# Kernel optimization log

Hardware: AMD Instinct MI355X
Metric: run time of the kernel (lower is better)

## Reference

```python
import jax, jax.numpy as jnp
import numpy as np

B, LQ, LK = 2, 2048, 77
DIM, XDIM = 320, 768
H, HD = 8, 40  # heads, head_dim; DIM == H*HD
FF = 4 * DIM  # GEGLU inner dim


def _ln(x, g, b, eps=1e-5):
    m = x.mean(-1, keepdims=True)
    v = ((x - m) ** 2).mean(-1, keepdims=True)
    return (x - m) * jax.lax.rsqrt(v + eps) * g + b


def _split_heads(x):  # [B,L,DIM] -> [B,H,L,HD]
    return x.reshape(x.shape[0], x.shape[1], H, HD).transpose(0, 2, 1, 3)


def _merge_heads(x):  # [B,H,L,HD] -> [B,L,DIM]
    return x.transpose(0, 2, 1, 3).reshape(x.shape[0], x.shape[2], H * HD)


def setup_inputs() -> dict:
    key = jax.random.key(0)
    ks = jax.random.split(key, 24)
    s = 0.02
    r = lambda i, shp: s * jax.random.normal(ks[i], shp, jnp.float32)
    return {
        "hidden_states": jax.random.normal(ks[0], (B, LQ, DIM), jnp.float32),
        "encoder_hidden_states": jax.random.normal(ks[1], (B, LK, XDIM), jnp.float32),
        # norm1 + self-attn (attn1)
        "ln1_g": jnp.ones((DIM,), jnp.float32), "ln1_b": jnp.zeros((DIM,), jnp.float32),
        "wq1": r(2, (DIM, DIM)), "wk1": r(3, (DIM, DIM)), "wv1": r(4, (DIM, DIM)),
        "wo1": r(5, (DIM, DIM)), "bo1": jnp.zeros((DIM,), jnp.float32),
        # norm2 + Hadamard cross-attn (attn2)
        "ln2_g": jnp.ones((DIM,), jnp.float32), "ln2_b": jnp.zeros((DIM,), jnp.float32),
        "wq2": r(6, (DIM, DIM)), "wk2": r(7, (XDIM, DIM)), "wvh": r(8, (DIM, DIM)),
        "wo2": r(9, (DIM, DIM)), "bo2": jnp.zeros((DIM,), jnp.float32),
        # norm3 + GEGLU feed-forward
        "ln3_g": jnp.ones((DIM,), jnp.float32), "ln3_b": jnp.zeros((DIM,), jnp.float32),
        "wff1": r(10, (DIM, 2 * FF)), "bff1": jnp.zeros((2 * FF,), jnp.float32),
        "wff2": r(11, (FF, DIM)), "bff2": jnp.zeros((DIM,), jnp.float32),
    }


def reference(hidden_states, encoder_hidden_states, ln1_g, ln1_b, wq1, wk1, wv1,
              wo1, bo1, ln2_g, ln2_b, wq2, wk2, wvh, wo2, bo2, ln3_g, ln3_b,
              wff1, bff1, wff2, bff2):
    scale = 1.0 / jnp.sqrt(jnp.asarray(HD, hidden_states.dtype))

    # ---- self-attention (SDPA semantics) ----
    h = _ln(hidden_states, ln1_g, ln1_b)
    q = _split_heads(h @ wq1)
    k = _split_heads(h @ wk1)
    v = _split_heads(h @ wv1)
    scores = jnp.einsum('bhqd,bhkd->bhqk', q, k) * scale
    w = jax.nn.softmax(scores, axis=-1)
    attn = jnp.einsum('bhqk,bhkd->bhqd', w, v)
    attn = _merge_heads(attn) @ wo1 + bo1
    hidden_states = hidden_states + attn

    # ---- Hadamard cross-attention: value comes from hidden_states (len Lq) ----
    h = _ln(hidden_states, ln2_g, ln2_b)
    q = _split_heads(h @ wq2)                     # [B,H,Lq,HD]
    k = _split_heads(encoder_hidden_states @ wk2) # [B,H,Lk,HD]
    vH = _split_heads(h @ wvh)                    # [B,H,Lq,HD]
    scores = jnp.einsum('bhqd,bhkd->bhqk', q, k) * scale
    w = jax.nn.softmax(scores, axis=-1)           # [B,H,Lq,Lk]
    # (w[...,None] * vH[...,None,:]).sum(-2) == vH * w.sum(-1, keepdims) (v indep of k)
    cross = vH * jnp.sum(w, axis=-1, keepdims=True)
    cross = _merge_heads(cross) @ wo2 + bo2
    hidden_states = hidden_states + cross

    # ---- GEGLU feed-forward ----
    h = _ln(hidden_states, ln3_g, ln3_b)
    proj = h @ wff1 + bff1
    x, gate = jnp.split(proj, 2, axis=-1)
    ff = (x * jax.nn.gelu(gate, approximate=False)) @ wff2 + bff2
    return hidden_states + ff
```

## Files before the change

### kernel.cpp

```cpp
#include <hip/hip_runtime.h>
#include <math.h>

#define DIM   320
#define HD    40
#define NH    8
#define LQ    2048
#define BATCH 2
#define MROWS 4096
#define FFD   1280
#define FF2   2560

#define KSPLIT 8
#define KCHUNK (LQ/KSPLIT)
#define KT     32
#define NT     (KCHUNK/KT)
#define NQROWS (BATCH*NH*LQ)

#define LSCALE (0.15811388300841897f * 1.4426950408889634f)

typedef unsigned short ushort_t;
typedef unsigned int u32;
using bf16x8 = __attribute__((ext_vector_type(8))) short;
using f32x4  = __attribute__((ext_vector_type(4))) float;

static __device__ inline ushort_t f2bf(float f) {
  union { float f; unsigned u; } x{f};
  unsigned r = x.u + 0x7FFFu + ((x.u >> 16) & 1u);
  return (ushort_t)(r >> 16);
}
static __device__ inline float bf2f(ushort_t h) {
  union { unsigned u; float f; } x; x.u = ((unsigned)h) << 16; return x.f;
}

__global__ __launch_bounds__(256) void ln_kernel(
    const float* __restrict__ X, const float* __restrict__ g,
    const float* __restrict__ bta, ushort_t* __restrict__ Y)
{
  int row  = blockIdx.x * 4 + (threadIdx.x >> 6);
  int lane = threadIdx.x & 63;
  const float* x = X + (size_t)row * DIM;
  float v[5];
  float s = 0.f;
#pragma unroll
  for (int i = 0; i < 5; ++i) { v[i] = x[lane + 64*i]; s += v[i]; }
#pragma unroll
  for (int off = 32; off >= 1; off >>= 1) s += __shfl_xor(s, off, 64);
  float mean = s * (1.0f/DIM);
  float sq = 0.f;
#pragma unroll
  for (int i = 0; i < 5; ++i) { float d = v[i] - mean; sq += d*d; }
#pragma unroll
  for (int off = 32; off >= 1; off >>= 1) sq += __shfl_xor(sq, off, 64);
  float rstd = rsqrtf(sq*(1.0f/DIM) + 1e-5f);
  ushort_t* y = Y + (size_t)row * DIM;
#pragma unroll
  for (int i = 0; i < 5; ++i) {
    int c = lane + 64*i;
    y[c] = f2bf((v[i]-mean)*rstd*g[c] + bta[c]);
  }
}

#define OFF_WQKVT 0
#define OFF_WO1T  (960*320)
#define OFF_WO2T  (OFF_WO1T + 320*320)
#define OFF_WFF1T (OFF_WO2T + 320*320)
#define OFF_WFF2T (OFF_WFF1T + 320*2560)
#define OFF_WVHB  (OFF_WFF2T + 1280*320)
#define WBF_TOTAL (OFF_WVHB + 320*320)

__global__ __launch_bounds__(256) void convw_kernel(
    const float* __restrict__ wq1, const float* __restrict__ wk1,
    const float* __restrict__ wv1, const float* __restrict__ wo1,
    const float* __restrict__ wo2, const float* __restrict__ wff1,
    const float* __restrict__ wff2, const float* __restrict__ wvh,
    ushort_t* __restrict__ dst)
{
  int e = blockIdx.y;
  const float* src; int K, N; size_t doff; int tr = 1; float scale = 1.f;
  switch (e) {
    case 0: src=wq1;  K=320;  N=320;  doff=OFF_WQKVT; scale=LSCALE; break;
    case 1: src=wk1;  K=320;  N=320;  doff=OFF_WQKVT + 320*320;  break;
    case 2: src=wv1;  K=320;  N=320;  doff=OFF_WQKVT + 2*320*320;break;
    case 3: src=wo1;  K=320;  N=320;  doff=OFF_WO1T;             break;
    case 4: src=wo2;  K=320;  N=320;  doff=OFF_WO2T;             break;
    case 5: src=wff1; K=320;  N=2560; doff=OFF_WFF1T;            break;
    case 6: src=wff2; K=1280; N=320;  doff=OFF_WFF2T;            break;
    default: src=wvh; K=320;  N=320;  doff=OFF_WVHB; tr=0;       break;
  }
  int ntN = N/32;
  int nt_total = (K/32)*ntN;
  int t = blockIdx.x;
  if (t >= nt_total) return;
  int kt = t / ntN, nt = t - kt*ntN;
  __shared__ float tile[32][33];
  int tx = threadIdx.x & 31, ty = threadIdx.x >> 5;
  ushort_t* d = dst + doff;
#pragma unroll
  for (int i = 0; i < 4; ++i) {
    int r = ty + 8*i;
    tile[r][tx] = src[(size_t)(kt*32+r)*N + nt*32+tx] * scale;
  }
  __syncthreads();
  if (tr) {
#pragma unroll
    for (int i = 0; i < 4; ++i) {
      int r = ty + 8*i;
      d[(size_t)(nt*32+r)*K + kt*32+tx] = f2bf(tile[tx][r]);
    }
  } else {
#pragma unroll
    for (int i = 0; i < 4; ++i) {
      int r = ty + 8*i;
      d[(size_t)(kt*32+r)*N + nt*32+tx] = f2bf(tile[r][tx]);
    }
  }
}

__global__ __launch_bounds__(256) void vt_kernel(
    const ushort_t* __restrict__ qkv, ushort_t* __restrict__ Vimg,
    ushort_t* __restrict__ Kimg)
{
  int bh = blockIdx.y;
  int kt = blockIdx.x;
  int b = bh >> 3, h = bh & 7;
  int tid = threadIdx.x;
  __shared__ ushort_t tile[64*42];

  const ushort_t* ksrc = qkv + (size_t)(b*LQ + kt*64)*960 + DIM + h*HD;
  ushort_t* kdst = Kimg + ((size_t)bh*64 + kt*2)*2048;
#pragma unroll
  for (int i = 0; i < 2; ++i) {
    int f = i*256 + tid;
    if (f < 320) {
      int r = f/5, s = f - 5*r;
      int t_ = r >> 5, rr = r & 31;
      int c = s ^ (rr & 7);
      *(uint4*)(kdst + (size_t)t_*2048 + rr*64 + c*8) =
          *(const uint4*)(ksrc + (size_t)r*960 + s*8);
    }
  }
  if (tid < 192) {
    int r = tid/3, s = tid - 3*r;
    int t_ = r >> 5, rr = r & 31;
    int c = (5+s) ^ (rr & 7);
    uint4 z = {0,0,0,0};
    *(uint4*)(kdst + (size_t)t_*2048 + rr*64 + c*8) = z;
  }

  const ushort_t* vsrc = qkv + (size_t)(b*LQ + kt*64)*960 + 2*DIM + h*HD;
#pragma unroll
  for (int i = 0; i < 5; ++i) {
    int f = i*256 + tid;
    int r = f/20, c2 = f - r*20;
    *(unsigned*)(tile + r*42 + c2*2) = *(const unsigned*)(vsrc + (size_t)r*960 + c2*2);
  }
  __syncthreads();
  ushort_t* vdst = Vimg + ((size_t)bh*64 + kt*2)*1536;
#pragma unroll
  for (int i = 0; i < 6; ++i) {
    int f = i*256 + tid;
    int dd = f >> 5, kk = f & 31;
    unsigned val = 0;
    if (dd < 40) {
      unsigned lo = tile[(kk*2)*42 + dd];
      unsigned hi = tile[(kk*2+1)*42 + dd];
      val = lo | (hi << 16);
    }
    int t_ = kk >> 4, p = kk & 15;
    int c = (p >> 2) ^ (dd & 3);
    *(unsigned*)(vdst + (size_t)t_*1536 + dd*32 + c*8 + (p&3)*2) = val;
  }
}

#define AST 72
__global__ __launch_bounds__(256) void mgemm(
    const ushort_t* __restrict__ A, int lda,
    const ushort_t* __restrict__ Bt, int ldb,
    const float* __restrict__ bias,
    const float* __restrict__ R,
    float* __restrict__ Cf, ushort_t* __restrict__ Cb, int ldc,
    int K)
{
  __shared__ ushort_t As[64*AST];
  __shared__ ushort_t Bs[64*AST];
  int tid = threadIdx.x;
  int w = tid >> 6, lane = tid & 63, quad = lane >> 4, n16 = lane & 15;
  int wm = w >> 1, wn = w & 1;
  int bm = blockIdx.y * 64, bn = blockIdx.x * 64;
  int sr = tid >> 2, sc = (tid & 3) << 4;
  const ushort_t* Ag = A  + (size_t)(bm + sr)*lda + sc;
  const ushort_t* Bg = Bt + (size_t)(bn + sr)*ldb + sc;

  f32x4 acc00 = {0.f,0.f,0.f,0.f}, acc01 = acc00, acc10 = acc00, acc11 = acc00;

  float4 av0 = *(const float4*)(Ag);
  float4 av1 = *(const float4*)(Ag + 8);
  float4 bv0 = *(const float4*)(Bg);
  float4 bv1 = *(const float4*)(Bg + 8);
  for (int k0 = 0; k0 < K; k0 += 64) {
    __syncthreads();
    *(float4*)(As + sr*AST + sc)     = av0;
    *(float4*)(As + sr*AST + sc + 8) = av1;
    *(float4*)(Bs + sr*AST + sc)     = bv0;
    *(float4*)(Bs + sr*AST + sc + 8) = bv1;
    __syncthreads();
    if (k0 + 64 < K) {
      av0 = *(const float4*)(Ag + k0 + 64);
      av1 = *(const float4*)(Ag + k0 + 72);
      bv0 = *(const float4*)(Bg + k0 + 64);
      bv1 = *(const float4*)(Bg + k0 + 72);
    }
#pragma unroll
    for (int kk = 0; kk < 64; kk += 32) {
      bf16x8 fa0 = *(const bf16x8*)(As + (wm*32 +      n16)*AST + kk + quad*8);
      bf16x8 fa1 = *(const bf16x8*)(As + (wm*32 + 16 + n16)*AST + kk + quad*8);
      bf16x8 fb0 = *(const bf16x8*)(Bs + (wn*32 +      n16)*AST + kk + quad*8);
      bf16x8 fb1 = *(const bf16x8*)(Bs + (wn*32 + 16 + n16)*AST + kk + quad*8);
      acc00 = __builtin_amdgcn_mfma_f32_16x16x32_bf16(fa0, fb0, acc00, 0,0,0);
      acc01 = __builtin_amdgcn_mfma_f32_16x16x32_bf16(fa0, fb1, acc01, 0,0,0);
      acc10 = __builtin_amdgcn_mfma_f32_16x16x32_bf16(fa1, fb0, acc10, 0,0,0);
      acc11 = __builtin_amdgcn_mfma_f32_16x16x32_bf16(fa1, fb1, acc11, 0,0,0);
    }
  }

  f32x4 accs[2][2] = {{acc00, acc01},{acc10, acc11}};
#pragma unroll
  for (int s = 0; s < 2; ++s)
#pragma unroll
    for (int t = 0; t < 2; ++t) {
      int c = bn + wn*32 + t*16 + n16;
      float bb = bias ? bias[c] : 0.f;
#pragma unroll
      for (int i = 0; i < 4; ++i) {
        int r = bm + wm*32 + s*16 + quad*4 + i;
        float v = accs[s][t][i] + bb;
        if (R)  v += R[(size_t)r*ldc + c];
        if (Cf) Cf[(size_t)r*ldc + c] = v;
        if (Cb) Cb[(size_t)r*ldc + c] = f2bf(v);
      }
    }
}

#define AS_STRIDE 40
__global__ __launch_bounds__(256) void mgemm128(
    const ushort_t* __restrict__ A, int lda,
    const ushort_t* __restrict__ Bt, int ldb,
    ushort_t* __restrict__ Cb, int ldc, int K)
{
  __shared__ ushort_t As[128*AS_STRIDE];
  __shared__ ushort_t Bs[64*AS_STRIDE];
  int tid = threadIdx.x;
  int w = tid >> 6, lane = tid & 63, quad = lane >> 4, n16 = lane & 15;
  int wm = w >> 1, wn = w & 1;
  int bm = blockIdx.y * 128, bn = blockIdx.x * 64;
  int ar = tid >> 1, ac = (tid & 1) << 4;
  int br = tid >> 2, bc = (tid & 3) << 3;
  const ushort_t* Ag = A  + (size_t)(bm + ar)*lda + ac;
  const ushort_t* Bg = Bt + (size_t)(bn + br)*ldb + bc;

  f32x4 acc[4][2];
#pragma unroll
  for (int s = 0; s < 4; ++s)
#pragma unroll
    for (int t = 0; t < 2; ++t) acc[s][t] = f32x4{0.f,0.f,0.f,0.f};

  float4 av0 = *(const float4*)(Ag);
  float4 av1 = *(const float4*)(Ag + 8);
  float4 bv  = *(const float4*)(Bg);
  for (int k0 = 0; k0 < K; k0 += 32) {
    __syncthreads();
    *(float4*)(As + ar*AS_STRIDE + ac)     = av0;
    *(float4*)(As + ar*AS_STRIDE + ac + 8) = av1;
    *(float4*)(Bs + br*AS_STRIDE + bc)     = bv;
    __syncthreads();
    if (k0 + 32 < K) {
      av0 = *(const float4*)(Ag + k0 + 32);
      av1 = *(const float4*)(Ag + k0 + 40);
      bv  = *(const float4*)(Bg + k0 + 32);
    }
    bf16x8 fa[4], fb[2];
#pragma unroll
    for (int s = 0; s < 4; ++s)
      fa[s] = *(const bf16x8*)(As + (wm*64 + s*16 + n16)*AS_STRIDE + quad*8);
#pragma unroll
    for (int t = 0; t < 2; ++t)
      fb[t] = *(const bf16x8*)(Bs + (wn*32 + t*16 + n16)*AS_STRIDE + quad*8);
#pragma unroll
    for (int s = 0; s < 4; ++s)
#pragma unroll
      for (int t = 0; t < 2; ++t)
        acc[s][t] = __builtin_amdgcn_mfma_f32_16x16x32_bf16(fa[s], fb[t], acc[s][t], 0,0,0);
  }

#pragma unroll
  for (int s = 0; s < 4; ++s)
#pragma unroll
    for (int t = 0; t < 2; ++t) {
      int c = bn + wn*32 + t*16 + n16;
#pragma unroll
      for (int i = 0; i < 4; ++i) {
        int r = bm + wm*64 + s*16 + quad*4 + i;
        Cb[(size_t)r*ldc + c] = f2bf(acc[s][t][i]);
      }
    }
}

__global__ __launch_bounds__(256) void ff1_geglu(
    const ushort_t* __restrict__ A, const ushort_t* __restrict__ Bt,
    const float* __restrict__ bias, ushort_t* __restrict__ Og)
{
  __shared__ ushort_t As[128*AS_STRIDE];
  __shared__ ushort_t Bxs[64*AS_STRIDE];
  __shared__ ushort_t Bgs[64*AS_STRIDE];
  int tid = threadIdx.x;
  int w = tid >> 6, lane = tid & 63, quad = lane >> 4, n16 = lane & 15;
  int wm = w >> 1, wn = w & 1;
  int bm = blockIdx.y * 128, bn = blockIdx.x * 64;
  int ar = tid >> 1, ac = (tid & 1) << 4;
  int br = tid >> 2, bc = (tid & 3) << 3;
  const ushort_t* Ag  = A  + (size_t)(bm + ar)*DIM + ac;
  const ushort_t* Bxg = Bt + (size_t)(bn + br)*DIM + bc;
  const ushort_t* Bgg = Bt + (size_t)(bn + FFD + br)*DIM + bc;

  f32x4 ax[4][2], ag[4][2];
#pragma unroll
  for (int s = 0; s < 4; ++s)
#pragma unroll
    for (int t = 0; t < 2; ++t) { ax[s][t] = f32x4{0.f,0.f,0.f,0.f}; ag[s][t] = ax[s][t]; }

  float4 av0 = *(const float4*)(Ag);
  float4 av1 = *(const float4*)(Ag + 8);
  float4 bxv = *(const float4*)(Bxg);
  float4 bgv = *(const float4*)(Bgg);
  for (int k0 = 0; k0 < DIM; k0 += 32) {
    __syncthreads();
    *(float4*)(As  + ar*AS_STRIDE + ac)     = av0;
    *(float4*)(As  + ar*AS_STRIDE + ac + 8) = av1;
    *(float4*)(Bxs + br*AS_STRIDE + bc)     = bxv;
    *(float4*)(Bgs + br*AS_STRIDE + bc)     = bgv;
    __syncthreads();
    if (k0 + 32 < DIM) {
      av0 = *(const float4*)(Ag  + k0 + 32);
      av1 = *(const float4*)(Ag  + k0 + 40);
      bxv = *(const float4*)(Bxg + k0 + 32);
      bgv = *(const float4*)(Bgg + k0 + 32);
    }
    bf16x8 fa[4], fx[2], fg[2];
#pragma unroll
    for (int s = 0; s < 4; ++s)
      fa[s] = *(const bf16x8*)(As + (wm*64 + s*16 + n16)*AS_STRIDE + quad*8);
#pragma unroll
    for (int t = 0; t < 2; ++t) {
      fx[t] = *(const bf16x8*)(Bxs + (wn*32 + t*16 + n16)*AS_STRIDE + quad*8);
      fg[t] = *(const bf16x8*)(Bgs + (wn*32 + t*16 + n16)*AS_STRIDE + quad*8);
    }
#pragma unroll
    for (int s = 0; s < 4; ++s)
#pragma unroll
      for (int t = 0; t < 2; ++t) {
        ax[s][t] = __builtin_amdgcn_mfma_f32_16x16x32_bf16(fa[s], fx[t], ax[s][t], 0,0,0);
        ag[s][t] = __builtin_amdgcn_mfma_f32_16x16x32_bf16(fa[s], fg[t], ag[s][t], 0,0,0);
      }
  }

  const float kk = 0.7071067811865476f;
#pragma unroll
  for (int s = 0; s < 4; ++s)
#pragma unroll
    for (int t = 0; t < 2; ++t) {
      int c = bn + wn*32 + t*16 + n16;
      float bx = bias[c], bg = bias[c + FFD];
#pragma unroll
      for (int i = 0; i < 4; ++i) {
        int r = bm + wm*64 + s*16 + quad*4 + i;
        float xx = ax[s][t][i] + bx;
        float gg = ag[s][t][i] + bg;
        Og[(size_t)r*FFD + c] = f2bf(xx * 0.5f * gg * (1.f + erff(gg * kk)));
      }
    }
}

#define TILE_K_SH 2048
#define TILE_V_SH 1536
#define TILE_SH   (TILE_K_SH + TILE_V_SH)

__global__ __launch_bounds__(256, 2) void attn_mfma(
    const ushort_t* __restrict__ qkv, const ushort_t* __restrict__ Kimg,
    const ushort_t* __restrict__ Vimg,
    float* __restrict__ Pl, ushort_t* __restrict__ Pacc)
{
  __shared__ ushort_t lds[2*TILE_SH];
  int tid  = threadIdx.x;
  int w    = tid >> 6;
  int lane = tid & 63;
  int quad = lane >> 4;
  int n16  = lane & 15;

  int blk  = blockIdx.x;
  int bh   = (blk & 7) | (((blk >> 3) & 1) << 3);
  int rest = blk >> 4;
  int qt   = rest & 15;
  int ks   = rest >> 4;
  int b = bh >> 3, h = bh & 7;

  const ushort_t* qrowa = qkv + (size_t)(b*LQ + qt*128 + w*32 + n16)*960 + h*HD;
  const ushort_t* qrowb = qrowa + 16*960;
  bf16x8 qf0a = *(const bf16x8*)(qrowa + quad*8);
  bf16x8 qf1a = *(const bf16x8*)(qrowa + 32);
  bf16x8 qf0b = *(const bf16x8*)(qrowb + quad*8);
  bf16x8 qf1b = *(const bf16x8*)(qrowb + 32);

  const ushort_t* Ktb = Kimg + ((size_t)bh*64 + ks*NT)*TILE_K_SH;
  const ushort_t* Vtb = Vimg + ((size_t)bh*64 + ks*NT)*TILE_V_SH;

  int swk0 = (quad ^ (n16 & 7)) << 3;
  int swk1 = ((quad + 4) ^ (n16 & 7)) << 3;
  int kof0 = n16*64 + swk0;
  int kof1 = n16*64 + swk1;
  int kof2 = (16+n16)*64 + swk0;
  int kof3 = (16+n16)*64 + swk1;
  int swv  = (quad ^ (n16 & 3)) << 3;
  int vof0 = n16*32 + swv;
  int vof1 = (16+n16)*32 + swv;
  int vof2 = (32+n16)*32 + swv;

  f32x4 o0a = {0.f,0.f,0.f,0.f}, o1a = o0a, o2a = o0a;
  f32x4 o0b = o0a, o1b = o0a, o2b = o0a;
  f32x4 la0a = o0a, la1a = o0a, la0b = o0a, la1b = o0a;

#define CVTPK(D, LO, HI) \
  asm("v_cvt_pk_bf16_f32 %0, %1, %2" : "=v"(D) : "v"(LO), "v"(HI))
#define PSWAP32(X, Y) \
  asm("v_permlane32_swap_b32 %0, %1" : "+v"(X), "+v"(Y))
#define PSWAP16(X, Y) \
  asm("v_permlane16_swap_b32 %0, %1" : "+v"(X), "+v"(Y))

#define STAGE(BUF, T) { \
  const ushort_t* ks_ = Ktb + (size_t)(T)*TILE_K_SH + w*512 + lane*8; \
  ushort_t* kd_ = lds + (BUF)*TILE_SH + w*512; \
  __builtin_amdgcn_global_load_lds( \
      (const __attribute__((address_space(1))) u32*)ks_, \
      (__attribute__((address_space(3))) u32*)kd_, 16, 0, 0); \
  if (w < 3) { \
    const ushort_t* vs_ = Vtb + (size_t)(T)*TILE_V_SH + w*512 + lane*8; \
    ushort_t* vd_ = lds + (BUF)*TILE_SH + TILE_K_SH + w*512; \
    __builtin_amdgcn_global_load_lds( \
        (const __attribute__((address_space(1))) u32*)vs_, \
        (__attribute__((address_space(3))) u32*)vd_, 16, 0, 0); \
  } }

#define HALF(Q0F, Q1F, LA0, LA1, FRAG) \
  bf16x8 FRAG; { \
  f32x4 st0 = {-8.f,-8.f,-8.f,-8.f}; f32x4 st1 = st0; \
  st0 = __builtin_amdgcn_mfma_f32_16x16x32_bf16(K00, Q0F, st0, 0,0,0); \
  st1 = __builtin_amdgcn_mfma_f32_16x16x32_bf16(K10, Q0F, st1, 0,0,0); \
  st0 = __builtin_amdgcn_mfma_f32_16x16x32_bf16(K01, Q1F, st0, 0,0,0); \
  st1 = __builtin_amdgcn_mfma_f32_16x16x32_bf16(K11, Q1F, st1, 0,0,0); \
  f32x4 p0, p1; \
  _Pragma("unroll") \
  for (int r = 0; r < 4; ++r) { p0[r] = exp2f(st0[r]); p1[r] = exp2f(st1[r]); } \
  LA0 += p0; LA1 += p1; \
  unsigned d0, d1, d2, d3; \
  CVTPK(d0, p0[0], p0[1]); CVTPK(d1, p0[2], p0[3]); \
  CVTPK(d2, p1[0], p1[1]); CVTPK(d3, p1[2], p1[3]); \
  PSWAP32(d0, d2); PSWAP16(d0, d2);   \
  PSWAP32(d1, d3); PSWAP16(d1, d3);   \
  union { unsigned u[4]; bf16x8 v; } fr_; \
  fr_.u[0] = d0; fr_.u[1] = d1; fr_.u[2] = d2; fr_.u[3] = d3; \
  FRAG = fr_.v; }

  STAGE(0, 0);
  __syncthreads();
  for (int t = 0; t < NT; ++t) {
    int buf = t & 1;
    if (t + 1 < NT) STAGE(buf^1, t+1);
    const ushort_t* Kb_ = lds + buf*TILE_SH;
    const ushort_t* Vb_ = Kb_ + TILE_K_SH;
    bf16x8 K00 = *(const bf16x8*)(Kb_ + kof0);
    bf16x8 K01 = *(const bf16x8*)(Kb_ + kof1);
    bf16x8 K10 = *(const bf16x8*)(Kb_ + kof2);
    bf16x8 K11 = *(const bf16x8*)(Kb_ + kof3);
    bf16x8 V0  = *(const bf16x8*)(Vb_ + vof0);
    bf16x8 V1  = *(const bf16x8*)(Vb_ + vof1);
    bf16x8 V2  = *(const bf16x8*)(Vb_ + vof2);
    HALF(qf0a, qf1a, la0a, la1a, fragA)
    HALF(qf0b, qf1b, la0b, la1b, fragB)
    o0a = __builtin_amdgcn_mfma_f32_16x16x32_bf16(fragA, V0, o0a, 0,0,0);
    o0b = __builtin_amdgcn_mfma_f32_16x16x32_bf16(fragB, V0, o0b, 0,0,0);
    o1a = __builtin_amdgcn_mfma_f32_16x16x32_bf16(fragA, V1, o1a, 0,0,0);
    o1b = __builtin_amdgcn_mfma_f32_16x16x32_bf16(fragB, V1, o1b, 0,0,0);
    o2a = __builtin_amdgcn_mfma_f32_16x16x32_bf16(fragA, V2, o2a, 0,0,0);
    o2b = __builtin_amdgcn_mfma_f32_16x16x32_bf16(fragB, V2, o2b, 0,0,0);
    __syncthreads();
  }
#undef STAGE
#undef HALF
#undef CVTPK
#undef PSWAP32
#undef PSWAP16
// ... 52 lines not shown
    ushort_t ob[8];
#pragma unroll
    for (int j = 0; j < 8; ++j) ob[j] = f2bf(acc[j]*inv);
    *(uint4*)(orow + u*8) = *(uint4*)ob;
  }
}

extern "C" void kernel_launch(void* const* d_in, const int* in_sizes, int n_in,
                              void* d_out, int out_size, void* d_ws, size_t ws_size,
                              hipStream_t stream) {
  const float* hidden = (const float*)d_in[0];
  const float* ln1_g = (const float*)d_in[2];
  const float* ln1_b = (const float*)d_in[3];
  const float* wq1   = (const float*)d_in[4];
  const float* wk1   = (const float*)d_in[5];
  const float* wv1   = (const float*)d_in[6];
  const float* wo1   = (const float*)d_in[7];
  const float* bo1   = (const float*)d_in[8];
  const float* ln2_g = (const float*)d_in[9];
  const float* ln2_b = (const float*)d_in[10];
  const float* wvh   = (const float*)d_in[13];
  const float* wo2   = (const float*)d_in[14];
  const float* bo2   = (const float*)d_in[15];
  const float* ln3_g = (const float*)d_in[16];
  const float* ln3_b = (const float*)d_in[17];
  const float* wff1  = (const float*)d_in[18];
  const float* bff1  = (const float*)d_in[19];
  const float* wff2  = (const float*)d_in[20];
  const float* bff2  = (const float*)d_in[21];
  float* out = (float*)d_out;

  ushort_t* wsu = (ushort_t*)d_ws;
  ushort_t* wbf   = wsu;
  ushort_t* lnb   = wbf + WBF_TOTAL;
  ushort_t* qkvb  = lnb + (size_t)MROWS*DIM;
  ushort_t* attnb = qkvb + (size_t)MROWS*3*DIM;
  ushort_t* gegb  = attnb + (size_t)MROWS*DIM;
  ushort_t* wct   = gegb + (size_t)MROWS*FFD;
  ushort_t* vtb   = wct + 320*320;
  ushort_t* kpb   = vtb + (size_t)16*64*1536;
  ushort_t* Pacc  = kpb + (size_t)16*64*2048;
  float* fws = (float*)(Pacc + (size_t)KSPLIT*NQROWS*40 + 64);
  float* h1   = fws;
  float* h2   = h1 + (size_t)MROWS*DIM;
  float* Pl   = h2 + (size_t)MROWS*DIM;

  dim3 t256(256);
  dim3 gconv(800, 8);
  dim3 gqkv(15, 32);
  dim3 g320(5, 64);
  dim3 gwc(5, 5);
  dim3 gffg(20, 32);
  dim3 gvt(32, 16);
  dim3 gattn(16*16*KSPLIT);

  convw_kernel<<<gconv, t256, 0, stream>>>(wq1, wk1, wv1, wo1, wo2, wff1, wff2, wvh, wbf);
  mgemm<<<gwc, t256, 0, stream>>>(wbf + OFF_WO2T, DIM, wbf + OFF_WVHB, DIM,
                                  nullptr, nullptr, nullptr, wct, DIM, DIM);

  ln_kernel<<<MROWS/4, t256, 0, stream>>>(hidden, ln1_g, ln1_b, lnb);
  mgemm128<<<gqkv, t256, 0, stream>>>(lnb, DIM, wbf + OFF_WQKVT, DIM,
                                      qkvb, 3*DIM, DIM);
  vt_kernel<<<gvt, t256, 0, stream>>>(qkvb, vtb, kpb);
  attn_mfma<<<gattn, t256, 0, stream>>>(qkvb, kpb, vtb, Pl, Pacc);
  attn_merge<<<NQROWS/256, t256, 0, stream>>>(Pl, Pacc, attnb);
  mgemm<<<g320, t256, 0, stream>>>(attnb, DIM, wbf + OFF_WO1T, DIM, bo1, hidden,
                                   h1, nullptr, DIM, DIM);

  ln_kernel<<<MROWS/4, t256, 0, stream>>>(h1, ln2_g, ln2_b, lnb);
  mgemm<<<g320, t256, 0, stream>>>(lnb, DIM, wct, DIM, bo2, h1,
                                   h2, nullptr, DIM, DIM);

  ln_kernel<<<MROWS/4, t256, 0, stream>>>(h2, ln3_g, ln3_b, lnb);
  ff1_geglu<<<gffg, t256, 0, stream>>>(lnb, wbf + OFF_WFF1T, bff1, gegb);
  mgemm<<<g320, t256, 0, stream>>>(gegb, FFD, wbf + OFF_WFF2T, FFD, bff2, h2,
                                   out, nullptr, DIM, FFD);
}
```

Before: 226.5 us.

## Fuse LayerNorm into GEMM prologues with atomic row statistics from epilogues

Removes the three standalone LayerNorm kernels. Row sum and sum-of-squares for the first LN are computed in an extra slice of the weight-conversion kernel. The residual GEMMs accumulate those statistics for the next LN via atomics in their epilogue, and the consuming GEMMs normalise fp32 input on the fly while staging A tiles into shared memory. This saves three launches and the bf16 LN buffer round trip, at the cost of reading fp32 activations (twice the bytes), recomputing the normalisation per N-tile, atomic contention, and a one-pass variance formula that is less numerically stable.

Result: slower. 251.0 us (+10.8%).

```diff
diff --git a/kernel.cpp b/kernel.cpp
--- a/kernel.cpp
+++ b/kernel.cpp
@@ -32,34 +32,6 @@
   union { unsigned u; float f; } x; x.u = ((unsigned)h) << 16; return x.f;
 }
 
-__global__ __launch_bounds__(256) void ln_kernel(
-    const float* __restrict__ X, const float* __restrict__ g,
-    const float* __restrict__ bta, ushort_t* __restrict__ Y)
-{
-  int row  = blockIdx.x * 4 + (threadIdx.x >> 6);
-  int lane = threadIdx.x & 63;
-  const float* x = X + (size_t)row * DIM;
-  float v[5];
-  float s = 0.f;
-#pragma unroll
-  for (int i = 0; i < 5; ++i) { v[i] = x[lane + 64*i]; s += v[i]; }
-#pragma unroll
-  for (int off = 32; off >= 1; off >>= 1) s += __shfl_xor(s, off, 64);
-  float mean = s * (1.0f/DIM);
-  float sq = 0.f;
-#pragma unroll
-  for (int i = 0; i < 5; ++i) { float d = v[i] - mean; sq += d*d; }
-#pragma unroll
-  for (int off = 32; off >= 1; off >>= 1) sq += __shfl_xor(sq, off, 64);
-  float rstd = rsqrtf(sq*(1.0f/DIM) + 1e-5f);
-  ushort_t* y = Y + (size_t)row * DIM;
-#pragma unroll
-  for (int i = 0; i < 5; ++i) {
-    int c = lane + 64*i;
-    y[c] = f2bf((v[i]-mean)*rstd*g[c] + bta[c]);
-  }
-}
-
 #define OFF_WQKVT 0
 #define OFF_WO1T  (960*320)
 #define OFF_WO2T  (OFF_WO1T + 320*320)
@@ -73,9 +45,30 @@
     const float* __restrict__ wv1, const float* __restrict__ wo1,
     const float* __restrict__ wo2, const float* __restrict__ wff1,
     const float* __restrict__ wff2, const float* __restrict__ wvh,
-    ushort_t* __restrict__ dst)
+    ushort_t* __restrict__ dst,
+    const float* __restrict__ hidden, float* __restrict__ stats0,
+    float* __restrict__ stats1, float* __restrict__ stats2)
 {
   int e = blockIdx.y;
+  if (e == 8) {
+    int row  = blockIdx.x * 4 + (threadIdx.x >> 6);
+    int lane = threadIdx.x & 63;
+    const float* x = hidden + (size_t)row * DIM;
+    float s = 0.f, q = 0.f;
+#pragma unroll
+    for (int i = 0; i < 5; ++i) { float v = x[lane + 64*i]; s += v; q += v*v; }
+#pragma unroll
+    for (int off = 32; off >= 1; off >>= 1) {
+      s += __shfl_xor(s, off, 64);
+      q += __shfl_xor(q, off, 64);
+    }
+    if (lane == 0) {
+      stats0[2*row] = s; stats0[2*row+1] = q;
+      stats1[2*row] = 0.f; stats1[2*row+1] = 0.f;
+      stats2[2*row] = 0.f; stats2[2*row+1] = 0.f;
+    }
+    return;
+  }
   const float* src; int K, N; size_t doff; int tr = 1; float scale = 1.f;
   switch (e) {
     case 0: src=wq1;  K=320;  N=320;  doff=OFF_WQKVT; scale=LSCALE; break;
@@ -173,13 +166,15 @@
 }
 
 #define AST 72
-__global__ __launch_bounds__(256) void mgemm(
-    const ushort_t* __restrict__ A, int lda,
+__global__ __launch_bounds__(256) void mgemm_x(
+    const ushort_t* __restrict__ Abf, const float* __restrict__ Xf, int lda,
+    const float* __restrict__ lnraw, const float* __restrict__ gi,
+    const float* __restrict__ bi,
     const ushort_t* __restrict__ Bt, int ldb,
     const float* __restrict__ bias,
     const float* __restrict__ R,
     float* __restrict__ Cf, ushort_t* __restrict__ Cb, int ldc,
-    int K)
+    int K, float* __restrict__ lnout)
 {
   __shared__ ushort_t As[64*AST];
   __shared__ ushort_t Bs[64*AST];
@@ -188,27 +183,55 @@
   int wm = w >> 1, wn = w & 1;
   int bm = blockIdx.y * 64, bn = blockIdx.x * 64;
   int sr = tid >> 2, sc = (tid & 3) << 4;
-  const ushort_t* Ag = A  + (size_t)(bm + sr)*lda + sc;
+  const ushort_t* Ag = Abf ? Abf + (size_t)(bm + sr)*lda + sc : nullptr;
+  const float*    Xg = Xf  ? Xf  + (size_t)(bm + sr)*lda + sc : nullptr;
   const ushort_t* Bg = Bt + (size_t)(bn + sr)*ldb + sc;
+  float m_ = 0.f, rs_ = 0.f;
+  if (Xf) {
+    float s = lnraw[2*(bm+sr)], q = lnraw[2*(bm+sr)+1];
+    m_  = s * (1.0f/DIM);
+    rs_ = rsqrtf(fmaxf(q*(1.0f/DIM) - m_*m_, 0.f) + 1e-5f);
+  }
 
   f32x4 acc00 = {0.f,0.f,0.f,0.f}, acc01 = acc00, acc10 = acc00, acc11 = acc00;
 
-  float4 av0 = *(const float4*)(Ag);
-  float4 av1 = *(const float4*)(Ag + 8);
-  float4 bv0 = *(const float4*)(Bg);
-  float4 bv1 = *(const float4*)(Bg + 8);
+  float4 ra0, ra1, ra2, ra3, rb0, rb1;
+  if (Abf) { ra0 = *(const float4*)(Ag); ra1 = *(const float4*)(Ag + 8); }
+  else     { ra0 = *(const float4*)(Xg);      ra1 = *(const float4*)(Xg + 4);
+             ra2 = *(const float4*)(Xg + 8);  ra3 = *(const float4*)(Xg + 12); }
+  rb0 = *(const float4*)(Bg);
+  rb1 = *(const float4*)(Bg + 8);
   for (int k0 = 0; k0 < K; k0 += 64) {
     __syncthreads();
-    *(float4*)(As + sr*AST + sc)     = av0;
-    *(float4*)(As + sr*AST + sc + 8) = av1;
-    *(float4*)(Bs + sr*AST + sc)     = bv0;
-    *(float4*)(Bs + sr*AST + sc + 8) = bv1;
+    if (Abf) {
+      *(float4*)(As + sr*AST + sc)     = ra0;
+      *(float4*)(As + sr*AST + sc + 8) = ra1;
+    } else {
+      float xs[16];
+      *(float4*)(xs)    = ra0; *(float4*)(xs+4)  = ra1;
+      *(float4*)(xs+8)  = ra2; *(float4*)(xs+12) = ra3;
+      float gg[16], bb[16];
+#pragma unroll
+      for (int u = 0; u < 4; ++u) {
+        *(float4*)(gg + 4*u) = *(const float4*)(gi + k0 + sc + 4*u);
+        *(float4*)(bb + 4*u) = *(const float4*)(bi + k0 + sc + 4*u);
+      }
+      ushort_t t16[16];
+#pragma unroll
+      for (int j = 0; j < 16; ++j)
+        t16[j] = f2bf((xs[j] - m_) * rs_ * gg[j] + bb[j]);
+      *(float4*)(As + sr*AST + sc)     = *(float4*)(t16);
+      *(float4*)(As + sr*AST + sc + 8) = *(float4*)(t16 + 8);
+    }
+    *(float4*)(Bs + sr*AST + sc)     = rb0;
+    *(float4*)(Bs + sr*AST + sc + 8) = rb1;
     __syncthreads();
     if (k0 + 64 < K) {
-      av0 = *(const float4*)(Ag + k0 + 64);
-      av1 = *(const float4*)(Ag + k0 + 72);
-      bv0 = *(const float4*)(Bg + k0 + 64);
-      bv1 = *(const float4*)(Bg + k0 + 72);
+      if (Abf) { ra0 = *(const float4*)(Ag + k0 + 64); ra1 = *(const float4*)(Ag + k0 + 72); }
+      else     { ra0 = *(const float4*)(Xg + k0 + 64); ra1 = *(const float4*)(Xg + k0 + 68);
+                 ra2 = *(const float4*)(Xg + k0 + 72); ra3 = *(const float4*)(Xg + k0 + 76); }
+      rb0 = *(const float4*)(Bg + k0 + 64);
+      rb1 = *(const float4*)(Bg + k0 + 72);
     }
 #pragma unroll
     for (int kk = 0; kk < 64; kk += 32) {
@@ -224,6 +247,7 @@
   }
 
   f32x4 accs[2][2] = {{acc00, acc01},{acc10, acc11}};
+  float vv[2][2][4];
 #pragma unroll
   for (int s = 0; s < 2; ++s)
 #pragma unroll
@@ -235,15 +259,37 @@
         int r = bm + wm*32 + s*16 + quad*4 + i;
         float v = accs[s][t][i] + bb;
         if (R)  v += R[(size_t)r*ldc + c];
+        vv[s][t][i] = v;
         if (Cf) Cf[(size_t)r*ldc + c] = v;
         if (Cb) Cb[(size_t)r*ldc + c] = f2bf(v);
       }
     }
+  if (lnout) {
+#pragma unroll
+    for (int s = 0; s < 2; ++s)
+#pragma unroll
+      for (int i = 0; i < 4; ++i) {
+        float cs = vv[s][0][i] + vv[s][1][i];
+        float cq = vv[s][0][i]*vv[s][0][i] + vv[s][1][i]*vv[s][1][i];
+#pragma unroll
+        for (int off = 1; off < 16; off <<= 1) {
+          cs += __shfl_xor(cs, off, 64);
+          cq += __shfl_xor(cq, off, 64);
+        }
+        if (n16 == 0) {
+          int r = bm + wm*32 + s*16 + quad*4 + i;
+          atomicAdd(&lnout[2*r],   cs);
+          atomicAdd(&lnout[2*r+1], cq);
+        }
+      }
+  }
 }
 
 #define AS_STRIDE 40
-__global__ __launch_bounds__(256) void mgemm128(
-    const ushort_t* __restrict__ A, int lda,
+__global__ __launch_bounds__(256) void mgemm128_ln(
+    const float* __restrict__ Xf, int lda,
+    const float* __restrict__ lnraw, const float* __restrict__ gi,
+    const float* __restrict__ bi,
     const ushort_t* __restrict__ Bt, int ldb,
     ushort_t* __restrict__ Cb, int ldc, int K)
 {
@@ -255,8 +301,11 @@
   int bm = blockIdx.y * 128, bn = blockIdx.x * 64;
   int ar = tid >> 1, ac = (tid & 1) << 4;
   int br = tid >> 2, bc = (tid & 3) << 3;
-  const ushort_t* Ag = A  + (size_t)(bm + ar)*lda + ac;
+  const float* Xg = Xf + (size_t)(bm + ar)*lda + ac;
   const ushort_t* Bg = Bt + (size_t)(bn + br)*ldb + bc;
+  float s_ = lnraw[2*(bm+ar)], q_ = lnraw[2*(bm+ar)+1];
+  float m_  = s_ * (1.0f/DIM);
+  float rs_ = rsqrtf(fmaxf(q_*(1.0f/DIM) - m_*m_, 0.f) + 1e-5f);
 
   f32x4 acc[4][2];
 #pragma unroll
@@ -264,18 +313,37 @@
 #pragma unroll
     for (int t = 0; t < 2; ++t) acc[s][t] = f32x4{0.f,0.f,0.f,0.f};
 
-  float4 av0 = *(const float4*)(Ag);
-  float4 av1 = *(const float4*)(Ag + 8);
+  float4 ra0 = *(const float4*)(Xg);
+  float4 ra1 = *(const float4*)(Xg + 4);
+  float4 ra2 = *(const float4*)(Xg + 8);
+  float4 ra3 = *(const float4*)(Xg + 12);
   float4 bv  = *(const float4*)(Bg);
   for (int k0 = 0; k0 < K; k0 += 32) {
     __syncthreads();
-    *(float4*)(As + ar*AS_STRIDE + ac)     = av0;
-    *(float4*)(As + ar*AS_STRIDE + ac + 8) = av1;
-    *(float4*)(Bs + br*AS_STRIDE + bc)     = bv;
+    {
+      float xs[16];
+      *(float4*)(xs)    = ra0; *(float4*)(xs+4)  = ra1;
+      *(float4*)(xs+8)  = ra2; *(float4*)(xs+12) = ra3;
+      float gg[16], bb[16];
+#pragma unroll
+      for (int u = 0; u < 4; ++u) {
+        *(float4*)(gg + 4*u) = *(const float4*)(gi + k0 + ac + 4*u);
+        *(float4*)(bb + 4*u) = *(const float4*)(bi + k0 + ac + 4*u);
+      }
+      ushort_t t16[16];
+#pragma unroll
+      for (int j = 0; j < 16; ++j)
+        t16[j] = f2bf((xs[j] - m_) * rs_ * gg[j] + bb[j]);
+      *(float4*)(As + ar*AS_STRIDE + ac)     = *(float4*)(t16);
+      *(float4*)(As + ar*AS_STRIDE + ac + 8) = *(float4*)(t16 + 8);
+    }
+    *(float4*)(Bs + br*AS_STRIDE + bc) = bv;
     __syncthreads();
     if (k0 + 32 < K) {
-      av0 = *(const float4*)(Ag + k0 + 32);
-      av1 = *(const float4*)(Ag + k0 + 40);
+      ra0 = *(const float4*)(Xg + k0 + 32);
+      ra1 = *(const float4*)(Xg + k0 + 36);
+      ra2 = *(const float4*)(Xg + k0 + 40);
+      ra3 = *(const float4*)(Xg + k0 + 44);
       bv  = *(const float4*)(Bg + k0 + 32);
     }
     bf16x8 fa[4], fb[2];
@@ -306,7 +374,9 @@
 }
 
 __global__ __launch_bounds__(256) void ff1_geglu(
-    const ushort_t* __restrict__ A, const ushort_t* __restrict__ Bt,
+    const float* __restrict__ Xf, const float* __restrict__ lnraw,
+    const float* __restrict__ gi, const float* __restrict__ bi,
+    const ushort_t* __restrict__ Bt,
     const float* __restrict__ bias, ushort_t* __restrict__ Og)
 {
   __shared__ ushort_t As[128*AS_STRIDE];
@@ -318,9 +388,12 @@
   int bm = blockIdx.y * 128, bn = blockIdx.x * 64;
   int ar = tid >> 1, ac = (tid & 1) << 4;
   int br = tid >> 2, bc = (tid & 3) << 3;
-  const ushort_t* Ag  = A  + (size_t)(bm + ar)*DIM + ac;
+  const float* Xg = Xf + (size_t)(bm + ar)*DIM + ac;
   const ushort_t* Bxg = Bt + (size_t)(bn + br)*DIM + bc;
   const ushort_t* Bgg = Bt + (size_t)(bn + FFD + br)*DIM + bc;
+  float s_ = lnraw[2*(bm+ar)], q_ = lnraw[2*(bm+ar)+1];
+  float m_  = s_ * (1.0f/DIM);
+  float rs_ = rsqrtf(fmaxf(q_*(1.0f/DIM) - m_*m_, 0.f) + 1e-5f);
 
   f32x4 ax[4][2], ag[4][2];
 #pragma unroll
@@ -328,20 +401,39 @@
 #pragma unroll
     for (int t = 0; t < 2; ++t) { ax[s][t] = f32x4{0.f,0.f,0.f,0.f}; ag[s][t] = ax[s][t]; }
 
-  float4 av0 = *(const float4*)(Ag);
-  float4 av1 = *(const float4*)(Ag + 8);
+  float4 ra0 = *(const float4*)(Xg);
+  float4 ra1 = *(const float4*)(Xg + 4);
+  float4 ra2 = *(const float4*)(Xg + 8);
+  float4 ra3 = *(const float4*)(Xg + 12);
   float4 bxv = *(const float4*)(Bxg);
   float4 bgv = *(const float4*)(Bgg);
   for (int k0 = 0; k0 < DIM; k0 += 32) {
     __syncthreads();
-    *(float4*)(As  + ar*AS_STRIDE + ac)     = av0;
-    *(float4*)(As  + ar*AS_STRIDE + ac + 8) = av1;
-    *(float4*)(Bxs + br*AS_STRIDE + bc)     = bxv;
-    *(float4*)(Bgs + br*AS_STRIDE + bc)     = bgv;
+    {
+      float xs[16];
+      *(float4*)(xs)    = ra0; *(float4*)(xs+4)  = ra1;
+      *(float4*)(xs+8)  = ra2; *(float4*)(xs+12) = ra3;
+      float gg[16], bb[16];
+#pragma unroll
+      for (int u = 0; u < 4; ++u) {
+        *(float4*)(gg + 4*u) = *(const float4*)(gi + k0 + ac + 4*u);
+        *(float4*)(bb + 4*u) = *(const float4*)(bi + k0 + ac + 4*u);
+      }
+      ushort_t t16[16];
+#pragma unroll
+      for (int j = 0; j < 16; ++j)
+        t16[j] = f2bf((xs[j] - m_) * rs_ * gg[j] + bb[j]);
+      *(float4*)(As + ar*AS_STRIDE + ac)     = *(float4*)(t16);
+      *(float4*)(As + ar*AS_STRIDE + ac + 8) = *(float4*)(t16 + 8);
+    }
+    *(float4*)(Bxs + br*AS_STRIDE + bc) = bxv;
+    *(float4*)(Bgs + br*AS_STRIDE + bc) = bgv;
     __syncthreads();
     if (k0 + 32 < DIM) {
-      av0 = *(const float4*)(Ag  + k0 + 32);
-      av1 = *(const float4*)(Ag  + k0 + 40);
+      ra0 = *(const float4*)(Xg + k0 + 32);
+      ra1 = *(const float4*)(Xg + k0 + 36);
+      ra2 = *(const float4*)(Xg + k0 + 40);
+      ra3 = *(const float4*)(Xg + k0 + 44);
       bxv = *(const float4*)(Bxg + k0 + 32);
       bgv = *(const float4*)(Bgg + k0 + 32);
     }
@@ -374,8 +466,8 @@
       for (int i = 0; i < 4; ++i) {
         int r = bm + wm*64 + s*16 + quad*4 + i;
         float xx = ax[s][t][i] + bx;
-        float gg = ag[s][t][i] + bg;
-        Og[(size_t)r*FFD + c] = f2bf(xx * 0.5f * gg * (1.f + erff(gg * kk)));
+        float gg2 = ag[s][t][i] + bg;
+        Og[(size_t)r*FFD + c] = f2bf(xx * 0.5f * gg2 * (1.f + erff(gg2 * kk)));
       }
     }
 }
@@ -463,8 +555,8 @@
   unsigned d0, d1, d2, d3; \
   CVTPK(d0, p0[0], p0[1]); CVTPK(d1, p0[2], p0[3]); \
   CVTPK(d2, p1[0], p1[1]); CVTPK(d3, p1[2], p1[3]); \
-  PSWAP32(d0, d2); PSWAP16(d0, d2);   \
-  PSWAP32(d1, d3); PSWAP16(d1, d3);   \
+  PSWAP32(d0, d2); PSWAP16(d0, d2); \
+  PSWAP32(d1, d3); PSWAP16(d1, d3); \
   union { unsigned u[4]; bf16x8 v; } fr_; \
   fr_.u[0] = d0; fr_.u[1] = d1; fr_.u[2] = d2; fr_.u[3] = d3; \
   FRAG = fr_.v; }
@@ -583,21 +675,23 @@
 
   ushort_t* wsu = (ushort_t*)d_ws;
   ushort_t* wbf   = wsu;
-  ushort_t* lnb   = wbf + WBF_TOTAL;
-  ushort_t* qkvb  = lnb + (size_t)MROWS*DIM;
+  ushort_t* qkvb  = wbf + WBF_TOTAL;
   ushort_t* attnb = qkvb + (size_t)MROWS*3*DIM;
   ushort_t* gegb  = attnb + (size_t)MROWS*DIM;
   ushort_t* wct   = gegb + (size_t)MROWS*FFD;
   ushort_t* vtb   = wct + 320*320;
   ushort_t* kpb   = vtb + (size_t)16*64*1536;
   ushort_t* Pacc  = kpb + (size_t)16*64*2048;
-  float* fws = (float*)(Pacc + (size_t)KSPLIT*NQROWS*40 + 64);
+  float* fws = (float*)((((uintptr_t)(Pacc + (size_t)KSPLIT*NQROWS*40)) + 255) & ~(uintptr_t)255);
   float* h1   = fws;
   float* h2   = h1 + (size_t)MROWS*DIM;
   float* Pl   = h2 + (size_t)MROWS*DIM;
+  float* stats0 = Pl + (size_t)KSPLIT*NQROWS;
+  float* stats1 = stats0 + 2*MROWS;
+  float* stats2 = stats1 + 2*MROWS;
 
   dim3 t256(256);
-  dim3 gconv(800, 8);
+  dim3 gconv(1024, 9);
   dim3 gqkv(15, 32);
   dim3 g320(5, 64);
   dim3 gwc(5, 5);
@@ -605,25 +699,32 @@
   dim3 gvt(32, 16);
   dim3 gattn(16*16*KSPLIT);
 
-  convw_kernel<<<gconv, t256, 0, stream>>>(wq1, wk1, wv1, wo1, wo2, wff1, wff2, wvh, wbf);
-  mgemm<<<gwc, t256, 0, stream>>>(wbf + OFF_WO2T, DIM, wbf + OFF_WVHB, DIM,
-                                  nullptr, nullptr, nullptr, wct, DIM, DIM);
-
-  ln_kernel<<<MROWS/4, t256, 0, stream>>>(hidden, ln1_g, ln1_b, lnb);
-  mgemm128<<<gqkv, t256, 0, stream>>>(lnb, DIM, wbf + OFF_WQKVT, DIM,
-                                      qkvb, 3*DIM, DIM);
+  convw_kernel<<<gconv, t256, 0, stream>>>(wq1, wk1, wv1, wo1, wo2, wff1, wff2,
+                                           wvh, wbf, hidden, stats0, stats1, stats2);
+  mgemm_x<<<gwc, t256, 0, stream>>>(wbf + OFF_WO2T, nullptr, DIM,
+                                    nullptr, nullptr, nullptr,
+                                    wbf + OFF_WVHB, DIM, nullptr, nullptr,
+                                    nullptr, wct, DIM, DIM, nullptr);
+
+  mgemm128_ln<<<gqkv, t256, 0, stream>>>(hidden, DIM, stats0, ln1_g, ln1_b,
+                                         wbf + OFF_WQKVT, DIM, qkvb, 3*DIM, DIM);
   vt_kernel<<<gvt, t256, 0, stream>>>(qkvb, vtb, kpb);
   attn_mfma<<<gattn, t256, 0, stream>>>(qkvb, kpb, vtb, Pl, Pacc);
   attn_merge<<<NQROWS/256, t256, 0, stream>>>(Pl, Pacc, attnb);
-  mgemm<<<g320, t256, 0, stream>>>(attnb, DIM, wbf + OFF_WO1T, DIM, bo1, hidden,
-                                   h1, nullptr, DIM, DIM);
-
-  ln_kernel<<<MROWS/4, t256, 0, stream>>>(h1, ln2_g, ln2_b, lnb);
-  mgemm<<<g320, t256, 0, stream>>>(lnb, DIM, wct, DIM, bo2, h1,
-                                   h2, nullptr, DIM, DIM);
-
-  ln_kernel<<<MROWS/4, t256, 0, stream>>>(h2, ln3_g, ln3_b, lnb);
-  ff1_geglu<<<gffg, t256, 0, stream>>>(lnb, wbf + OFF_WFF1T, bff1, gegb);
-  mgemm<<<g320, t256, 0, stream>>>(gegb, FFD, wbf + OFF_WFF2T, FFD, bff2, h2,
-                                   out, nullptr, DIM, FFD);
-}
+  mgemm_x<<<g320, t256, 0, stream>>>(attnb, nullptr, DIM,
+                                     nullptr, nullptr, nullptr,
+                                     wbf + OFF_WO1T, DIM, bo1, hidden,
+                                     h1, nullptr, DIM, DIM, stats1);
+
+  mgemm_x<<<g320, t256, 0, stream>>>(nullptr, h1, DIM,
+                                     stats1, ln2_g, ln2_b,
+                                     wct, DIM, bo2, h1,
+                                     h2, nullptr, DIM, DIM, stats2);
+
+  ff1_geglu<<<gffg, t256, 0, stream>>>(h2, stats2, ln3_g, ln3_b,
+                                       wbf + OFF_WFF1T, bff1, gegb);
+  mgemm_x<<<g320, t256, 0, stream>>>(gegb, nullptr, FFD,
+                                     nullptr, nullptr, nullptr,
+                                     wbf + OFF_WFF2T, FFD, bff2, h2,
+                                     out, nullptr, DIM, FFD, nullptr);
+}
```

## Fuse K/V swizzled layout writes into QKV GEGEMM epilogue and drop vt_kernel

Applied to the files above, without the earlier changes.

The QKV projection GEMM epilogue now writes Q to a compact buffer and scatters K and V straight into the swizzled tile images the attention kernel reads. This removes the separate vt_kernel pass and its round-trip of the QKV buffer through global memory. Zeroing of the K padding columns moves into an extra y-slice of the weight conversion kernel. The cost is scattered 2-byte and 4-byte stores in the GEMM epilogue instead of coalesced row writes.

New measurement: 225.8 us. No clear change (-0.3%).

```diff
diff --git a/kernel.cpp b/kernel.cpp
--- a/kernel.cpp
+++ b/kernel.cpp
@@ -73,9 +73,20 @@
     const float* __restrict__ wv1, const float* __restrict__ wo1,
     const float* __restrict__ wo2, const float* __restrict__ wff1,
     const float* __restrict__ wff2, const float* __restrict__ wvh,
-    ushort_t* __restrict__ dst)
+    ushort_t* __restrict__ dst, ushort_t* __restrict__ Kimg)
 {
   int e = blockIdx.y;
+  if (e == 8) {
+    int f = blockIdx.x*256 + threadIdx.x;
+    if (f < 98304) {
+      int g3 = f/3, cidx = f - 3*g3;
+      int rr = g3 & 31, tile = (g3 >> 5) & 63, bh = g3 >> 11;
+      uint4 z = {0,0,0,0};
+      *(uint4*)(Kimg + ((size_t)(bh*64 + tile))*2048 + rr*64
+                + (((5+cidx) ^ (rr&7)) << 3)) = z;
+    }
+    return;
+  }
   const float* src; int K, N; size_t doff; int tr = 1; float scale = 1.f;
   switch (e) {
     case 0: src=wq1;  K=320;  N=320;  doff=OFF_WQKVT; scale=LSCALE; break;
@@ -113,62 +124,6 @@
       int r = ty + 8*i;
       d[(size_t)(kt*32+r)*N + nt*32+tx] = f2bf(tile[r][tx]);
     }
-  }
-}
-
-__global__ __launch_bounds__(256) void vt_kernel(
-    const ushort_t* __restrict__ qkv, ushort_t* __restrict__ Vimg,
-    ushort_t* __restrict__ Kimg)
-{
-  int bh = blockIdx.y;
-  int kt = blockIdx.x;
-  int b = bh >> 3, h = bh & 7;
-  int tid = threadIdx.x;
-  __shared__ ushort_t tile[64*42];
-
-  const ushort_t* ksrc = qkv + (size_t)(b*LQ + kt*64)*960 + DIM + h*HD;
-  ushort_t* kdst = Kimg + ((size_t)bh*64 + kt*2)*2048;
-#pragma unroll
-  for (int i = 0; i < 2; ++i) {
-    int f = i*256 + tid;
-    if (f < 320) {
-      int r = f/5, s = f - 5*r;
-      int t_ = r >> 5, rr = r & 31;
-      int c = s ^ (rr & 7);
-      *(uint4*)(kdst + (size_t)t_*2048 + rr*64 + c*8) =
-          *(const uint4*)(ksrc + (size_t)r*960 + s*8);
-    }
-  }
-  if (tid < 192) {
-    int r = tid/3, s = tid - 3*r;
-    int t_ = r >> 5, rr = r & 31;
-    int c = (5+s) ^ (rr & 7);
-    uint4 z = {0,0,0,0};
-    *(uint4*)(kdst + (size_t)t_*2048 + rr*64 + c*8) = z;
-  }
-
-  const ushort_t* vsrc = qkv + (size_t)(b*LQ + kt*64)*960 + 2*DIM + h*HD;
-#pragma unroll
-  for (int i = 0; i < 5; ++i) {
-    int f = i*256 + tid;
-    int r = f/20, c2 = f - r*20;
-    *(unsigned*)(tile + r*42 + c2*2) = *(const unsigned*)(vsrc + (size_t)r*960 + c2*2);
-  }
-  __syncthreads();
-  ushort_t* vdst = Vimg + ((size_t)bh*64 + kt*2)*1536;
-#pragma unroll
-  for (int i = 0; i < 6; ++i) {
-    int f = i*256 + tid;
-    int dd = f >> 5, kk = f & 31;
-    unsigned val = 0;
-    if (dd < 40) {
-      unsigned lo = tile[(kk*2)*42 + dd];
-      unsigned hi = tile[(kk*2+1)*42 + dd];
-      val = lo | (hi << 16);
-    }
-    int t_ = kk >> 4, p = kk & 15;
-    int c = (p >> 2) ^ (dd & 3);
-    *(unsigned*)(vdst + (size_t)t_*1536 + dd*32 + c*8 + (p&3)*2) = val;
   }
 }
 
@@ -242,10 +197,10 @@
 }
 
 #define AS_STRIDE 40
-__global__ __launch_bounds__(256) void mgemm128(
-    const ushort_t* __restrict__ A, int lda,
-    const ushort_t* __restrict__ Bt, int ldb,
-    ushort_t* __restrict__ Cb, int ldc, int K)
+__global__ __launch_bounds__(256) void mgemm128_qkv(
+    const ushort_t* __restrict__ A, const ushort_t* __restrict__ Bt,
+    ushort_t* __restrict__ Qb, ushort_t* __restrict__ Kimg,
+    ushort_t* __restrict__ Vimg)
 {
   __shared__ ushort_t As[128*AS_STRIDE];
   __shared__ ushort_t Bs[64*AS_STRIDE];
@@ -255,8 +210,8 @@
   int bm = blockIdx.y * 128, bn = blockIdx.x * 64;
   int ar = tid >> 1, ac = (tid & 1) << 4;
   int br = tid >> 2, bc = (tid & 3) << 3;
-  const ushort_t* Ag = A  + (size_t)(bm + ar)*lda + ac;
-  const ushort_t* Bg = Bt + (size_t)(bn + br)*ldb + bc;
+  const ushort_t* Ag = A  + (size_t)(bm + ar)*DIM + ac;
+  const ushort_t* Bg = Bt + (size_t)(bn + br)*DIM + bc;
 
   f32x4 acc[4][2];
 #pragma unroll
@@ -267,13 +222,13 @@
   float4 av0 = *(const float4*)(Ag);
   float4 av1 = *(const float4*)(Ag + 8);
   float4 bv  = *(const float4*)(Bg);
-  for (int k0 = 0; k0 < K; k0 += 32) {
+  for (int k0 = 0; k0 < DIM; k0 += 32) {
     __syncthreads();
     *(float4*)(As + ar*AS_STRIDE + ac)     = av0;
     *(float4*)(As + ar*AS_STRIDE + ac + 8) = av1;
     *(float4*)(Bs + br*AS_STRIDE + bc)     = bv;
     __syncthreads();
-    if (k0 + 32 < K) {
+    if (k0 + 32 < DIM) {
       av0 = *(const float4*)(Ag + k0 + 32);
       av1 = *(const float4*)(Ag + k0 + 40);
       bv  = *(const float4*)(Bg + k0 + 32);
@@ -292,17 +247,57 @@
         acc[s][t] = __builtin_amdgcn_mfma_f32_16x16x32_bf16(fa[s], fb[t], acc[s][t], 0,0,0);
   }
 
-#pragma unroll
-  for (int s = 0; s < 4; ++s)
+  int b8 = (bm >> 11) << 3;
+  if (bn < 320) {
+#pragma unroll
+    for (int s = 0; s < 4; ++s)
+#pragma unroll
+      for (int t = 0; t < 2; ++t) {
+        int c = bn + wn*32 + t*16 + n16;
+#pragma unroll
+        for (int i = 0; i < 4; ++i) {
+          int r = bm + wm*64 + s*16 + quad*4 + i;
+          Qb[(size_t)r*320 + c] = f2bf(acc[s][t][i]);
+        }
+      }
+  } else if (bn < 640) {
 #pragma unroll
     for (int t = 0; t < 2; ++t) {
-      int c = bn + wn*32 + t*16 + n16;
-#pragma unroll
-      for (int i = 0; i < 4; ++i) {
-        int r = bm + wm*64 + s*16 + quad*4 + i;
-        Cb[(size_t)r*ldc + c] = f2bf(acc[s][t][i]);
+      int c = bn + wn*32 + t*16 + n16 - 320;
+      int hK = c / 40, d = c - hK*40;
+      ushort_t* kb = Kimg + ((size_t)(b8 + hK))*64*2048
+                   + (((d >> 3) ^ 0) << 3) + (d & 7);
+#pragma unroll
+      for (int s = 0; s < 4; ++s)
+#pragma unroll
+        for (int i = 0; i < 4; ++i) {
+          int r = bm + wm*64 + s*16 + quad*4 + i;
+          int l = r & 2047, tl = l >> 5, rr = l & 31;
+          Kimg[((size_t)((b8 + hK)*64 + tl))*2048 + rr*64
+               + (((d >> 3) ^ (rr & 7)) << 3) + (d & 7)] = f2bf(acc[s][t][i]);
+        }
+      (void)kb;
+    }
+  } else {
+#pragma unroll
+    for (int t = 0; t < 2; ++t) {
+      int c = bn + wn*32 + t*16 + n16 - 640;
+      int hV = c / 40, d = c - hV*40;
+#pragma unroll
+      for (int s = 0; s < 4; ++s) {
+        int l0 = (bm + wm*64 + s*16 + quad*4) & 2047;
+        int tl = l0 >> 5, p0 = (l0 & 31) >> 1;
+        ushort_t* vb = Vimg + ((size_t)((b8 + hV)*64 + tl))*1536 + d*32;
+#pragma unroll
+        for (int j = 0; j < 2; ++j) {
+          int p = p0 + j;
+          unsigned val = (unsigned)f2bf(acc[s][t][2*j])
+                       | ((unsigned)f2bf(acc[s][t][2*j+1]) << 16);
+          *(unsigned*)(vb + (((p >> 2) ^ (d & 3)) << 3) + ((p & 3) << 1)) = val;
+        }
       }
     }
+  }
 }
 
 __global__ __launch_bounds__(256) void ff1_geglu(
@@ -385,7 +380,7 @@
 #define TILE_SH   (TILE_K_SH + TILE_V_SH)
 
 __global__ __launch_bounds__(256, 2) void attn_mfma(
-    const ushort_t* __restrict__ qkv, const ushort_t* __restrict__ Kimg,
+    const ushort_t* __restrict__ Qb, const ushort_t* __restrict__ Kimg,
     const ushort_t* __restrict__ Vimg,
     float* __restrict__ Pl, ushort_t* __restrict__ Pacc)
 {
@@ -403,8 +398,8 @@
   int ks   = rest >> 4;
   int b = bh >> 3, h = bh & 7;
 
-  const ushort_t* qrowa = qkv + (size_t)(b*LQ + qt*128 + w*32 + n16)*960 + h*HD;
-  const ushort_t* qrowb = qrowa + 16*960;
+  const ushort_t* qrowa = Qb + (size_t)(b*LQ + qt*128 + w*32 + n16)*320 + h*HD;
+  const ushort_t* qrowb = qrowa + 16*320;
   bf16x8 qf0a = *(const bf16x8*)(qrowa + quad*8);
   bf16x8 qf1a = *(const bf16x8*)(qrowa + 32);
   bf16x8 qf0b = *(const bf16x8*)(qrowb + quad*8);
@@ -463,8 +458,8 @@
   unsigned d0, d1, d2, d3; \
   CVTPK(d0, p0[0], p0[1]); CVTPK(d1, p0[2], p0[3]); \
   CVTPK(d2, p1[0], p1[1]); CVTPK(d3, p1[2], p1[3]); \
-  PSWAP32(d0, d2); PSWAP16(d0, d2);   \
-  PSWAP32(d1, d3); PSWAP16(d1, d3);   \
+  PSWAP32(d0, d2); PSWAP16(d0, d2); \
+  PSWAP32(d1, d3); PSWAP16(d1, d3); \
   union { unsigned u[4]; bf16x8 v; } fr_; \
   fr_.u[0] = d0; fr_.u[1] = d1; fr_.u[2] = d2; fr_.u[3] = d3; \
   FRAG = fr_.v; }
@@ -584,36 +579,34 @@
   ushort_t* wsu = (ushort_t*)d_ws;
   ushort_t* wbf   = wsu;
   ushort_t* lnb   = wbf + WBF_TOTAL;
-  ushort_t* qkvb  = lnb + (size_t)MROWS*DIM;
-  ushort_t* attnb = qkvb + (size_t)MROWS*3*DIM;
+  ushort_t* Qb    = lnb + (size_t)MROWS*DIM;
+  ushort_t* attnb = Qb + (size_t)MROWS*DIM;
   ushort_t* gegb  = attnb + (size_t)MROWS*DIM;
   ushort_t* wct   = gegb + (size_t)MROWS*FFD;
   ushort_t* vtb   = wct + 320*320;
   ushort_t* kpb   = vtb + (size_t)16*64*1536;
   ushort_t* Pacc  = kpb + (size_t)16*64*2048;
-  float* fws = (float*)(Pacc + (size_t)KSPLIT*NQROWS*40 + 64);
+  float* fws = (float*)((((uintptr_t)(Pacc + (size_t)KSPLIT*NQROWS*40)) + 255) & ~(uintptr_t)255);
   float* h1   = fws;
   float* h2   = h1 + (size_t)MROWS*DIM;
   float* Pl   = h2 + (size_t)MROWS*DIM;
 
   dim3 t256(256);
-  dim3 gconv(800, 8);
+  dim3 gconv(1024, 9);
   dim3 gqkv(15, 32);
   dim3 g320(5, 64);
   dim3 gwc(5, 5);
   dim3 gffg(20, 32);
-  dim3 gvt(32, 16);
   dim3 gattn(16*16*KSPLIT);
 
-  convw_kernel<<<gconv, t256, 0, stream>>>(wq1, wk1, wv1, wo1, wo2, wff1, wff2, wvh, wbf);
+  convw_kernel<<<gconv, t256, 0, stream>>>(wq1, wk1, wv1, wo1, wo2, wff1, wff2,
+                                           wvh, wbf, kpb);
   mgemm<<<gwc, t256, 0, stream>>>(wbf + OFF_WO2T, DIM, wbf + OFF_WVHB, DIM,
                                   nullptr, nullptr, nullptr, wct, DIM, DIM);
 
   ln_kernel<<<MROWS/4, t256, 0, stream>>>(hidden, ln1_g, ln1_b, lnb);
-  mgemm128<<<gqkv, t256, 0, stream>>>(lnb, DIM, wbf + OFF_WQKVT, DIM,
-                                      qkvb, 3*DIM, DIM);
-  vt_kernel<<<gvt, t256, 0, stream>>>(qkvb, vtb, kpb);
-  attn_mfma<<<gattn, t256, 0, stream>>>(qkvb, kpb, vtb, Pl, Pacc);
+  mgemm128_qkv<<<gqkv, t256, 0, stream>>>(lnb, wbf + OFF_WQKVT, Qb, kpb, vtb);
+  attn_mfma<<<gattn, t256, 0, stream>>>(Qb, kpb, vtb, Pl, Pacc);
   attn_merge<<<NQROWS/256, t256, 0, stream>>>(Pl, Pacc, attnb);
   mgemm<<<g320, t256, 0, stream>>>(attnb, DIM, wbf + OFF_WO1T, DIM, bo1, hidden,
                                    h1, nullptr, DIM, DIM);
```
